# Kernel tuning notes

Hardware: AMD Instinct MI355X
Metric: run time of the kernel (lower is better)

## Reference

```python
import jax, jax.numpy as jnp
import numpy as np

GROUPS = 4
RATIO = 2


def setup_inputs() -> dict:
    key = jax.random.key(0)
    k1, k2, k3 = jax.random.split(key, 3)
    B, C, H, W = 16, 256, 64, 64
    c_out = 2 * GROUPS * RATIO ** 2  # 32
    x = jax.random.normal(k1, (B, C, H, W), dtype=jnp.float32)
    # offset conv: normal_init std=0.001 (full 1x1 conv)
    w_off = jax.random.normal(k2, (c_out, C), dtype=jnp.float32) * 0.001
    b_off = jnp.zeros((c_out,), dtype=jnp.float32)
    # scope conv: grouped 1x1 (groups=4); init is zeros in the module, use tiny
    # random values so sigmoid != exactly 0.5 and the path is exercised
    w_scope = jax.random.normal(k3, (GROUPS, c_out // GROUPS, C // GROUPS), dtype=jnp.float32) * 0.001
    b_scope = jnp.zeros((c_out,), dtype=jnp.float32)
    return {"x": x, "w_off": w_off, "b_off": b_off, "w_scope": w_scope, "b_scope": b_scope}


def _pixel_shuffle(t, r):
    B, C, H, W = t.shape
    Co = C // (r * r)
    t = t.reshape(B, Co, r, r, H, W)
    t = t.transpose(0, 1, 4, 2, 5, 3)  # B, Co, H, r, W, r
    return t.reshape(B, Co, H * r, W * r)


def _bilinear_border(img, ix, iy):
    # img: (c, H, W); ix, iy: (Ho, Wo) pixel coords in input space
    c, H, W = img.shape
    ix = jnp.clip(ix, 0.0, W - 1.0)  # border padding: clamp coordinate
    iy = jnp.clip(iy, 0.0, H - 1.0)
    x0f = jnp.floor(ix)
    y0f = jnp.floor(iy)
    wx = ix - x0f
    wy = iy - y0f
    x0 = jnp.clip(x0f.astype(jnp.int32), 0, W - 1)
    x1 = jnp.clip(x0 + 1, 0, W - 1)
    y0 = jnp.clip(y0f.astype(jnp.int32), 0, H - 1)
    y1 = jnp.clip(y0 + 1, 0, H - 1)
    v00 = img[:, y0, x0]
    v01 = img[:, y0, x1]
    v10 = img[:, y1, x0]
    v11 = img[:, y1, x1]
    return (v00 * (1 - wy) * (1 - wx) + v01 * (1 - wy) * wx
            + v10 * wy * (1 - wx) + v11 * wy * wx)


def reference(x, w_off, b_off, w_scope, b_scope):
    B, C, H, W = x.shape
    g, r = GROUPS, RATIO
    # offset 1x1 conv
    off = jnp.einsum('bihw,oi->bohw', x, w_off) + b_off[None, :, None, None]
    # grouped scope 1x1 conv + sigmoid scaling
    xgc = x.reshape(B, g, C // g, H, W)
    sc = jnp.einsum('bgihw,goi->bgohw', xgc, w_scope).reshape(B, -1, H, W)
    sc = sc + b_scope[None, :, None, None]
    off = jax.nn.sigmoid(sc) * 0.5 * off
    # pixel shuffle to (B, 2*g, Ho, Wo)
    off = _pixel_shuffle(off, r)
    Ho, Wo = H * r, W * r
    # rearrange: x 'b (c grp) h w -> (b grp) c h w'; offset 'b (grp two) h w -> (b grp) h w two'
    cg = C // g
    xg = x.reshape(B, cg, g, H, W).transpose(0, 2, 1, 3, 4).reshape(B * g, cg, H, W)
    og = off.reshape(B, g, 2, Ho, Wo).transpose(0, 1, 3, 4, 2).reshape(B * g, Ho, Wo, 2)
    # sampling grid: centers + offset, normalized by (Wo, Ho), align_corners=False
    posx = jnp.linspace(0.5, Wo - 0.5, Wo, dtype=x.dtype)[None, :]   # (1, Wo)
    posy = jnp.linspace(0.5, Ho - 0.5, Ho, dtype=x.dtype)[:, None]   # (Ho, 1)
    gx = 2.0 * (posx + og[..., 0]) / Wo - 1.0  # (B*g, Ho, Wo)
    gy = 2.0 * (posy + og[..., 1]) / Ho - 1.0
    # unnormalize (align_corners=False): pix = ((g+1)*size - 1) / 2
    ix = ((gx + 1.0) * W - 1.0) * 0.5
    iy = ((gy + 1.0) * H - 1.0) * 0.5
    out = jax.vmap(_bilinear_border)(xg, ix, iy)  # (B*g, cg, Ho, Wo)
    # rearrange back: '(b grp) c h w -> b (c grp) h w'
    out = out.reshape(B, g, cg, Ho, Wo).transpose(0, 2, 1, 3, 4).reshape(B, C, Ho, Wo)
    return out
```

## Files before the change

kernel.cpp:

```cpp
#include <hip/hip_runtime.h>
#include <math.h>

#define B_   16
#define C_   256
#define H_   64
#define W_   64
#define G_   4
#define HO_  128
#define WO_  128
#define HW_  (H_ * W_)
#define HOWO_ (HO_ * WO_)

__constant__ float wconst[8 * 32 * 40];

__global__ __launch_bounds__(256) void prep_kernel(
    const float* __restrict__ w_off,
    const float* __restrict__ w_scope,
    float* __restrict__ wout)
{
    const int k = blockIdx.x * 256 + threadIdx.x;
    if (k >= 8 * 32 * 40) return;
    const int q  = k % 40;
    const int r  = k / 40;
    const int i2 = r & 31;
    const int u  = r >> 5;
    const int v  = u & 3;
    const int hi = u >> 2;
    const int i  = 64 * v + 32 * hi + i2;
    float val;
    if (q < 32) val = w_off[q * 256 + i];
    else        val = w_scope[v * 512 + (q - 32) * 64 + 32 * hi + i2];
    wout[k] = val;
}

__global__ __launch_bounds__(512, 8) void fused_kernel(
    const float* __restrict__ x,
    const float* __restrict__ b_off,
    const float* __restrict__ b_scope,
    float* __restrict__ out)
{
    __shared__ float4 red[4][8][64];
    __shared__ float4 aux[8][64];

    const int tid = threadIdx.x;
    const int u   = __builtin_amdgcn_readfirstlane(tid >> 6);
    const int w   = tid & 63;

    const int bid = ((blockIdx.x & 7) << 7) | (blockIdx.x >> 3);
    const int h   = bid & 63;
    const int b   = bid >> 6;

    const int v   = u & 3;
    const int hi  = u >> 2;

    const float* xq = x + (size_t)b * C_ * HW_ +
                      (size_t)(64 * v + 32 * hi) * HW_ + h * W_ + w;
    const int wbase0 = u * (32 * 40);

    float offp[32];
    float scp[8];
#pragma unroll
    for (int j = 0; j < 32; ++j) offp[j] = 0.f;
#pragma unroll
    for (int j = 0; j < 8; ++j) scp[j] = 0.f;

#pragma unroll 4
    for (int i2 = 0; i2 < 32; ++i2) {
        const float xv = xq[(size_t)i2 * HW_];
        const int wb = wbase0 + i2 * 40;
#pragma unroll
        for (int j = 0; j < 32; ++j) offp[j] += xv * wconst[wb + j];
#pragma unroll
        for (int j = 0; j < 8; ++j)  scp[j] += xv * wconst[wb + 32 + j];
    }

    if (hi) {
#pragma unroll
        for (int j = 0; j < 8; ++j)
            red[v][j][w] = make_float4(offp[4 * j + 0], offp[4 * j + 1],
                                       offp[4 * j + 2], offp[4 * j + 3]);
        aux[2 * v + 0][w] = make_float4(scp[0], scp[1], scp[2], scp[3]);
        aux[2 * v + 1][w] = make_float4(scp[4], scp[5], scp[6], scp[7]);
    }
    __syncthreads();
    if (!hi) {
#pragma unroll
        for (int j = 0; j < 8; ++j) {
            const float4 p = red[v][j][w];
            offp[4 * j + 0] += p.x; offp[4 * j + 1] += p.y;
            offp[4 * j + 2] += p.z; offp[4 * j + 3] += p.w;
        }
        const float4 s0 = aux[2 * v + 0][w];
        const float4 s1 = aux[2 * v + 1][w];
        scp[0] += s0.x; scp[1] += s0.y; scp[2] += s0.z; scp[3] += s0.w;
        scp[4] += s1.x; scp[5] += s1.y; scp[6] += s1.z; scp[7] += s1.w;
#pragma unroll
        for (int j = 0; j < 8; ++j)
            red[v][j][w] = make_float4(offp[4 * j + 0], offp[4 * j + 1],
                                       offp[4 * j + 2], offp[4 * j + 3]);
    }
    __syncthreads();
    if (!hi) {
        float4 a = make_float4(0.f, 0.f, 0.f, 0.f);
        float4 c = make_float4(0.f, 0.f, 0.f, 0.f);
#pragma unroll
        for (int tt = 0; tt < 4; ++tt) {
            const float4 pa = red[tt][2 * v + 0][w];
            const float4 pc = red[tt][2 * v + 1][w];
            a.x += pa.x; a.y += pa.y; a.z += pa.z; a.w += pa.w;
            c.x += pc.x; c.y += pc.y; c.z += pc.z; c.w += pc.w;
        }
        const float ao[8] = {a.x, a.y, a.z, a.w, c.x, c.y, c.z, c.w};
        float f[8];
#pragma unroll
        for (int j = 0; j < 8; ++j) {
            const float offv = ao[j] + b_off[8 * v + j];
            const float scv  = scp[j] + b_scope[8 * v + j];
            f[j] = offv * 0.5f / (1.f + expf(-scv));
        }
#pragma unroll
        for (int r1 = 0; r1 < 2; ++r1) {
            const float hoF = (float)(2 * h + r1);
            float ix0 = ((float)(2 * w + 0) - 0.5f + f[2 * r1 + 0]) * 0.5f;
            float iy0 = (hoF - 0.5f + f[4 + 2 * r1 + 0]) * 0.5f;
            float ix1 = ((float)(2 * w + 1) - 0.5f + f[2 * r1 + 1]) * 0.5f;
            float iy1 = (hoF - 0.5f + f[4 + 2 * r1 + 1]) * 0.5f;
            ix0 = fminf(fmaxf(ix0, 0.f), (float)(W_ - 1));
            iy0 = fminf(fmaxf(iy0, 0.f), (float)(H_ - 1));
            ix1 = fminf(fmaxf(ix1, 0.f), (float)(W_ - 1));
            iy1 = fminf(fmaxf(iy1, 0.f), (float)(H_ - 1));
            aux[2 * v + r1][w] = make_float4(ix0, iy0, ix1, iy1);
        }
    }
    __syncthreads();

    const int wo = tid & 127;
    const int z  = (tid >> 7) & 1;
    const int gh = tid >> 8;
    const int ho = 2 * h + z;

    const float2* cbase = (const float2*)&aux[0][0];
    const float* xb0 = x + (size_t)b * C_ * HW_;
    float* ob0 = out + (size_t)b * C_ * HOWO_ + ho * WO_ + wo;

#pragma unroll
    for (int gg = 0; gg < 2; ++gg) {
        const int g = 2 * gh + gg;
        const float2 c = cbase[(g * 2 + z) * 128 + wo];
        const float ix = c.x, iy = c.y;

        const float x0f = floorf(ix);
        const float y0f = floorf(iy);
        const float wx = ix - x0f;
        const float wy = iy - y0f;
        int x0 = (int)x0f;
        int y0 = (int)y0f;
        x0 = max(0, min(x0, W_ - 1));
        y0 = max(0, min(y0, H_ - 1));
        const int x1 = min(x0 + 1, W_ - 1);
        const int y1 = min(y0 + 1, H_ - 1);

        const float w00 = (1.f - wy) * (1.f - wx);
        const float w01 = (1.f - wy) * wx;
        const float w10 = wy * (1.f - wx);
        const float w11 = wy * wx;

        const int p00 = y0 * W_ + x0;
        const int p01 = y0 * W_ + x1;
        const int p10 = y1 * W_ + x0;
        const int p11 = y1 * W_ + x1;

        const float* xb = xb0 + (size_t)g * HW_;
        float* ob = ob0 + (size_t)g * HOWO_;

#pragma unroll 4
        for (int cc = 0; cc < 64; ++cc) {
            const float* pl = xb + (size_t)cc * 4 * HW_;
            const float val = pl[p00] * w00 + pl[p01] * w01 +
                              pl[p10] * w10 + pl[p11] * w11;
            __builtin_nontemporal_store(val, &ob[(size_t)cc * 4 * HOWO_]);
        }
    }
}

extern "C" void kernel_launch(void* const* d_in, const int* in_sizes, int n_in,
                              void* d_out, int out_size, void* d_ws, size_t ws_size,
                              hipStream_t stream) {
    const float* x       = (const float*)d_in[0];
    const float* w_off   = (const float*)d_in[1];
    const float* b_off   = (const float*)d_in[2];
    const float* w_scope = (const float*)d_in[3];
    const float* b_scope = (const float*)d_in[4];
    float* out = (float*)d_out;

    void* wsym = nullptr;
    (void)hipGetSymbolAddress(&wsym, HIP_SYMBOL(wconst));

    prep_kernel<<<dim3(40), 256, 0, stream>>>(w_off, w_scope, (float*)wsym);
    fused_kernel<<<dim3(B_ * H_), 512, 0, stream>>>(x, b_off, b_scope, out);
}
```

Before: 88.51 us.

## Process two input rows per block and prefetch next row's channels

Each block now handles two consecutive input rows, halving the grid to 512 blocks. All 32 channel values for a row are loaded into registers up front, and the next row's values are fetched after the current row's conv accumulation so the load overlaps later work. Launch bounds drop to 4 waves per SIMD to make room for the extra registers. The intent is better latency hiding and less per-block overhead, at the cost of lower occupancy and fewer blocks to spread across CUs.

```diff
diff --git a/kernel.cpp b/kernel.cpp
--- a/kernel.cpp
+++ b/kernel.cpp
@@ -33,7 +33,7 @@
     wout[k] = val;
 }
 
-__global__ __launch_bounds__(512, 8) void fused_kernel(
+__global__ __launch_bounds__(512, 4) void fused_kernel(
     const float* __restrict__ x,
     const float* __restrict__ b_off,
     const float* __restrict__ b_scope,
@@ -46,139 +46,157 @@
     const int u   = __builtin_amdgcn_readfirstlane(tid >> 6);
     const int w   = tid & 63;
 
-    const int bid = ((blockIdx.x & 7) << 7) | (blockIdx.x >> 3);
-    const int h   = bid & 63;
-    const int b   = bid >> 6;
+    const int xcd = blockIdx.x & 7;
+    const int j   = blockIdx.x >> 3;
+    const int b   = 2 * xcd + (j >> 5);
+    const int h0  = 2 * (j & 31);
 
     const int v   = u & 3;
     const int hi  = u >> 2;
 
     const float* xq = x + (size_t)b * C_ * HW_ +
-                      (size_t)(64 * v + 32 * hi) * HW_ + h * W_ + w;
+                      (size_t)(64 * v + 32 * hi) * HW_ + h0 * W_ + w;
     const int wbase0 = u * (32 * 40);
 
-    float offp[32];
-    float scp[8];
-#pragma unroll
-    for (int j = 0; j < 32; ++j) offp[j] = 0.f;
-#pragma unroll
-    for (int j = 0; j < 8; ++j) scp[j] = 0.f;
+    float xv[32];
+#pragma unroll
+    for (int i2 = 0; i2 < 32; ++i2) xv[i2] = xq[(size_t)i2 * HW_];
+
+#pragma unroll
+    for (int t = 0; t < 2; ++t) {
+        const int h = h0 + t;
+
+        float offp[32];
+        float scp[8];
+#pragma unroll
+        for (int jj = 0; jj < 32; ++jj) offp[jj] = 0.f;
+#pragma unroll
+        for (int jj = 0; jj < 8; ++jj) scp[jj] = 0.f;
+
+#pragma unroll
+        for (int i2 = 0; i2 < 32; ++i2) {
+            const float xvv = xv[i2];
+            const int wb = wbase0 + i2 * 40;
+#pragma unroll
+            for (int jj = 0; jj < 32; ++jj) offp[jj] += xvv * wconst[wb + jj];
+#pragma unroll
+            for (int jj = 0; jj < 8; ++jj)  scp[jj] += xvv * wconst[wb + 32 + jj];
+        }
+
+        if (t == 0) {
+#pragma unroll
+            for (int i2 = 0; i2 < 32; ++i2)
+                xv[i2] = xq[(size_t)i2 * HW_ + W_];
+        }
+
+        __syncthreads();
+
+        if (hi) {
+#pragma unroll
+            for (int jj = 0; jj < 8; ++jj)
+                red[v][jj][w] = make_float4(offp[4 * jj + 0], offp[4 * jj + 1],
+                                            offp[4 * jj + 2], offp[4 * jj + 3]);
+            aux[2 * v + 0][w] = make_float4(scp[0], scp[1], scp[2], scp[3]);
+            aux[2 * v + 1][w] = make_float4(scp[4], scp[5], scp[6], scp[7]);
+        }
+        __syncthreads();
+        if (!hi) {
+#pragma unroll
+            for (int jj = 0; jj < 8; ++jj) {
+                const float4 p = red[v][jj][w];
+                offp[4 * jj + 0] += p.x; offp[4 * jj + 1] += p.y;
+                offp[4 * jj + 2] += p.z; offp[4 * jj + 3] += p.w;
+            }
+            const float4 s0 = aux[2 * v + 0][w];
+            const float4 s1 = aux[2 * v + 1][w];
+            scp[0] += s0.x; scp[1] += s0.y; scp[2] += s0.z; scp[3] += s0.w;
+            scp[4] += s1.x; scp[5] += s1.y; scp[6] += s1.z; scp[7] += s1.w;
+#pragma unroll
+            for (int jj = 0; jj < 8; ++jj)
+                red[v][jj][w] = make_float4(offp[4 * jj + 0], offp[4 * jj + 1],
+                                            offp[4 * jj + 2], offp[4 * jj + 3]);
+        }
+        __syncthreads();
+        if (!hi) {
+            float4 a = make_float4(0.f, 0.f, 0.f, 0.f);
+            float4 c = make_float4(0.f, 0.f, 0.f, 0.f);
+#pragma unroll
+            for (int tt = 0; tt < 4; ++tt) {
+                const float4 pa = red[tt][2 * v + 0][w];
+                const float4 pc = red[tt][2 * v + 1][w];
+                a.x += pa.x; a.y += pa.y; a.z += pa.z; a.w += pa.w;
+                c.x += pc.x; c.y += pc.y; c.z += pc.z; c.w += pc.w;
+            }
+            const float ao[8] = {a.x, a.y, a.z, a.w, c.x, c.y, c.z, c.w};
+            float f[8];
+#pragma unroll
+            for (int jj = 0; jj < 8; ++jj) {
+                const float offv = ao[jj] + b_off[8 * v + jj];
+                const float scv  = scp[jj] + b_scope[8 * v + jj];
+                f[jj] = offv * 0.5f / (1.f + expf(-scv));
+            }
+#pragma unroll
+            for (int r1 = 0; r1 < 2; ++r1) {
+                const float hoF = (float)(2 * h + r1);
+                float ix0 = ((float)(2 * w + 0) - 0.5f + f[2 * r1 + 0]) * 0.5f;
+                float iy0 = (hoF - 0.5f + f[4 + 2 * r1 + 0]) * 0.5f;
+                float ix1 = ((float)(2 * w + 1) - 0.5f + f[2 * r1 + 1]) * 0.5f;
+                float iy1 = (hoF - 0.5f + f[4 + 2 * r1 + 1]) * 0.5f;
+                ix0 = fminf(fmaxf(ix0, 0.f), (float)(W_ - 1));
+                iy0 = fminf(fmaxf(iy0, 0.f), (float)(H_ - 1));
+                ix1 = fminf(fmaxf(ix1, 0.f), (float)(W_ - 1));
+                iy1 = fminf(fmaxf(iy1, 0.f), (float)(H_ - 1));
+                aux[2 * v + r1][w] = make_float4(ix0, iy0, ix1, iy1);
+            }
+        }
+        __syncthreads();
+
+        const int wo = tid & 127;
+        const int z  = (tid >> 7) & 1;
+        const int gh = tid >> 8;
+        const int ho = 2 * h + z;
+
+        const float2* cbase = (const float2*)&aux[0][0];
+        const float* xb0 = x + (size_t)b * C_ * HW_;
+        float* ob0 = out + (size_t)b * C_ * HOWO_ + ho * WO_ + wo;
+
+#pragma unroll
+        for (int gg = 0; gg < 2; ++gg) {
+            const int g = 2 * gh + gg;
+            const float2 c = cbase[(g * 2 + z) * 128 + wo];
+            const float ix = c.x, iy = c.y;
+
+            const float x0f = floorf(ix);
+            const float y0f = floorf(iy);
+            const float wx = ix - x0f;
+            const float wy = iy - y0f;
+            int x0 = (int)x0f;
+            int y0 = (int)y0f;
+            x0 = max(0, min(x0, W_ - 1));
+            y0 = max(0, min(y0, H_ - 1));
+            const int x1 = min(x0 + 1, W_ - 1);
+            const int y1 = min(y0 + 1, H_ - 1);
+
+            const float w00 = (1.f - wy) * (1.f - wx);
+            const float w01 = (1.f - wy) * wx;
+            const float w10 = wy * (1.f - wx);
+            const float w11 = wy * wx;
+
+            const int p00 = y0 * W_ + x0;
+            const int p01 = y0 * W_ + x1;
+            const int p10 = y1 * W_ + x0;
+            const int p11 = y1 * W_ + x1;
+
+            const float* xb = xb0 + (size_t)g * HW_;
+            float* ob = ob0 + (size_t)g * HOWO_;
 
 #pragma unroll 4
-    for (int i2 = 0; i2 < 32; ++i2) {
-        const float xv = xq[(size_t)i2 * HW_];
-        const int wb = wbase0 + i2 * 40;
-#pragma unroll
-        for (int j = 0; j < 32; ++j) offp[j] += xv * wconst[wb + j];
-#pragma unroll
-        for (int j = 0; j < 8; ++j)  scp[j] += xv * wconst[wb + 32 + j];
-    }
-
-    if (hi) {
-#pragma unroll
-        for (int j = 0; j < 8; ++j)
-            red[v][j][w] = make_float4(offp[4 * j + 0], offp[4 * j + 1],
-                                       offp[4 * j + 2], offp[4 * j + 3]);
-        aux[2 * v + 0][w] = make_float4(scp[0], scp[1], scp[2], scp[3]);
-        aux[2 * v + 1][w] = make_float4(scp[4], scp[5], scp[6], scp[7]);
-    }
-    __syncthreads();
-    if (!hi) {
-#pragma unroll
-        for (int j = 0; j < 8; ++j) {
-            const float4 p = red[v][j][w];
-            offp[4 * j + 0] += p.x; offp[4 * j + 1] += p.y;
-            offp[4 * j + 2] += p.z; offp[4 * j + 3] += p.w;
-        }
-        const float4 s0 = aux[2 * v + 0][w];
-        const float4 s1 = aux[2 * v + 1][w];
-        scp[0] += s0.x; scp[1] += s0.y; scp[2] += s0.z; scp[3] += s0.w;
-        scp[4] += s1.x; scp[5] += s1.y; scp[6] += s1.z; scp[7] += s1.w;
-#pragma unroll
-        for (int j = 0; j < 8; ++j)
-            red[v][j][w] = make_float4(offp[4 * j + 0], offp[4 * j + 1],
-                                       offp[4 * j + 2], offp[4 * j + 3]);
-    }
-    __syncthreads();
-    if (!hi) {
-        float4 a = make_float4(0.f, 0.f, 0.f, 0.f);
-        float4 c = make_float4(0.f, 0.f, 0.f, 0.f);
-#pragma unroll
-        for (int tt = 0; tt < 4; ++tt) {
-            const float4 pa = red[tt][2 * v + 0][w];
-            const float4 pc = red[tt][2 * v + 1][w];
-            a.x += pa.x; a.y += pa.y; a.z += pa.z; a.w += pa.w;
-            c.x += pc.x; c.y += pc.y; c.z += pc.z; c.w += pc.w;
-        }
-        const float ao[8] = {a.x, a.y, a.z, a.w, c.x, c.y, c.z, c.w};
-        float f[8];
-#pragma unroll
-        for (int j = 0; j < 8; ++j) {
-            const float offv = ao[j] + b_off[8 * v + j];
-            const float scv  = scp[j] + b_scope[8 * v + j];
-            f[j] = offv * 0.5f / (1.f + expf(-scv));
-        }
-#pragma unroll
-        for (int r1 = 0; r1 < 2; ++r1) {
-            const float hoF = (float)(2 * h + r1);
-            float ix0 = ((float)(2 * w + 0) - 0.5f + f[2 * r1 + 0]) * 0.5f;
-            float iy0 = (hoF - 0.5f + f[4 + 2 * r1 + 0]) * 0.5f;
-            float ix1 = ((float)(2 * w + 1) - 0.5f + f[2 * r1 + 1]) * 0.5f;
-            float iy1 = (hoF - 0.5f + f[4 + 2 * r1 + 1]) * 0.5f;
-            ix0 = fminf(fmaxf(ix0, 0.f), (float)(W_ - 1));
-            iy0 = fminf(fmaxf(iy0, 0.f), (float)(H_ - 1));
-            ix1 = fminf(fmaxf(ix1, 0.f), (float)(W_ - 1));
-            iy1 = fminf(fmaxf(iy1, 0.f), (float)(H_ - 1));
-            aux[2 * v + r1][w] = make_float4(ix0, iy0, ix1, iy1);
-        }
-    }
-    __syncthreads();
-
-    const int wo = tid & 127;
-    const int z  = (tid >> 7) & 1;
-    const int gh = tid >> 8;
-    const int ho = 2 * h + z;
-
-    const float2* cbase = (const float2*)&aux[0][0];
-    const float* xb0 = x + (size_t)b * C_ * HW_;
-    float* ob0 = out + (size_t)b * C_ * HOWO_ + ho * WO_ + wo;
-
-#pragma unroll
-    for (int gg = 0; gg < 2; ++gg) {
-        const int g = 2 * gh + gg;
-        const float2 c = cbase[(g * 2 + z) * 128 + wo];
-        const float ix = c.x, iy = c.y;
-
-        const float x0f = floorf(ix);
-        const float y0f = floorf(iy);
-        const float wx = ix - x0f;
-        const float wy = iy - y0f;
-        int x0 = (int)x0f;
-        int y0 = (int)y0f;
-        x0 = max(0, min(x0, W_ - 1));
-        y0 = max(0, min(y0, H_ - 1));
-        const int x1 = min(x0 + 1, W_ - 1);
-        const int y1 = min(y0 + 1, H_ - 1);
-
-        const float w00 = (1.f - wy) * (1.f - wx);
-        const float w01 = (1.f - wy) * wx;
-        const float w10 = wy * (1.f - wx);
-        const float w11 = wy * wx;
-
-        const int p00 = y0 * W_ + x0;
-        const int p01 = y0 * W_ + x1;
-        const int p10 = y1 * W_ + x0;
-        const int p11 = y1 * W_ + x1;
-
-        const float* xb = xb0 + (size_t)g * HW_;
-        float* ob = ob0 + (size_t)g * HOWO_;
-
-#pragma unroll 4
-        for (int cc = 0; cc < 64; ++cc) {
-            const float* pl = xb + (size_t)cc * 4 * HW_;
-            const float val = pl[p00] * w00 + pl[p01] * w01 +
-                              pl[p10] * w10 + pl[p11] * w11;
-            __builtin_nontemporal_store(val, &ob[(size_t)cc * 4 * HOWO_]);
+            for (int cc = 0; cc < 64; ++cc) {
+                const float* pl = xb + (size_t)cc * 4 * HW_;
+                const float val = pl[p00] * w00 + pl[p01] * w01 +
+                                  pl[p10] * w10 + pl[p11] * w11;
+                __builtin_nontemporal_store(val, &ob[(size_t)cc * 4 * HOWO_]);
+            }
         }
     }
 }
@@ -197,5 +215,5 @@
     (void)hipGetSymbolAddress(&wsym, HIP_SYMBOL(wconst));
 
     prep_kernel<<<dim3(40), 256, 0, stream>>>(w_off, w_scope, (float*)wsym);
-    fused_kernel<<<dim3(B_ * H_), 512, 0, stream>>>(x, b_off, b_scope, out);
+    fused_kernel<<<dim3(512), 512, 0, stream>>>(x, b_off, b_scope, out);
 }
```

After: 97.85 us. 10.5% more time.
